# Kernel tuning notes

Measured on AMD Instinct MI355X. Metric: run time of the kernel, lower is better.

The kernel has to match this reference:

```python
import jax, jax.numpy as jnp
import numpy as np

EMB = 1024
HEADS = 16
S = EMB // HEADS  # per-head dim


def setup_inputs() -> dict:
    key = jax.random.key(0)
    ks = jax.random.split(key, 6)
    x = jax.random.normal(ks[0], (4, 2048, EMB), dtype=jnp.float32)
    # torch nn.Linear(s, s, bias=False): weight [out, in], y = x @ W.T
    Wk = jax.random.normal(ks[1], (S, S), dtype=jnp.float32) * (1.0 / np.sqrt(S))
    Wq = jax.random.normal(ks[2], (S, S), dtype=jnp.float32) * (1.0 / np.sqrt(S))
    Wv = jax.random.normal(ks[3], (S, S), dtype=jnp.float32) * (1.0 / np.sqrt(S))
    # unifyHeads: Linear(heads*s, emb) with bias
    Wu = jax.random.normal(ks[4], (EMB, EMB), dtype=jnp.float32) * (1.0 / np.sqrt(EMB))
    bu = jax.random.normal(ks[5], (EMB,), dtype=jnp.float32) * 0.01
    return {"x": x, "Wk": Wk, "Wq": Wq, "Wv": Wv, "Wu": Wu, "bu": bu}


def reference(x, Wk, Wq, Wv, Wu, bu):
    b, t, e = x.shape
    h, s = HEADS, S
    x4 = x.reshape(b, t, h, s)
    # per-head narrow projections (y = x @ W.T)
    k = jnp.einsum('bths,os->bhto', x4, Wk)  # [b,h,t,s]
    q = jnp.einsum('bths,os->bhto', x4, Wq)
    v = jnp.einsum('bths,os->bhto', x4, Wv)
    scale = e ** 0.25
    q = q / scale
    k = k / scale
    dot = jnp.einsum('bhqs,bhks->bhqk', q, k)  # [b,h,t,t]
    attn = jax.nn.softmax(dot, axis=-1)
    out = jnp.einsum('bhqk,bhks->bhqs', attn, v)  # [b,h,t,s]
    out = out.transpose(0, 2, 1, 3).reshape(b, t, h * s)
    return out @ Wu.T + bu
```

## Files before the change

### kernel.cpp

```cpp
#include <hip/hip_runtime.h>
#include <hip/hip_bf16.h>

#define BB 4
#define TT 2048
#define HH 16
#define SS 64
#define EE 1024

typedef __attribute__((ext_vector_type(8))) short short8;
typedef __attribute__((ext_vector_type(4))) short short4v;
typedef __attribute__((ext_vector_type(4))) float float4v;
typedef unsigned long long ull;

__device__ inline short f2bf(float f) {
    union { __hip_bfloat16 h; short s; } u;
    u.h = __float2bfloat16(f);
    return u.s;
}

__device__ inline unsigned pack_bf(float lo, float hi) {
    return ((unsigned)(unsigned short)f2bf(hi) << 16) | (unsigned short)f2bf(lo);
}

__device__ inline unsigned pack_trunc(float lo, float hi) {
    unsigned a = __builtin_bit_cast(unsigned, lo);
    unsigned b = __builtin_bit_cast(unsigned, hi);
    return (b & 0xFFFF0000u) | (a >> 16);
}

__device__ inline float4v mfma16(short8 a, short8 b, float4v c) {
    return __builtin_amdgcn_mfma_f32_16x16x32_bf16(a, b, c, 0, 0, 0);
}

#define LDSP(p) ((__attribute__((address_space(3))) void*)(p))
#define GLBP(p) ((const __attribute__((address_space(1))) void*)(p))

__global__ __launch_bounds__(256) void k_qkv(
    const float* __restrict__ x, const float* __restrict__ Wk,
    const float* __restrict__ Wq, const float* __restrict__ Wv,
    short* __restrict__ qb, short* __restrict__ kb, short* __restrict__ vb)
{
    __shared__ __attribute__((aligned(16))) short lw[3][64][72];
    const int tid = threadIdx.x;
    const float sq = 0.21233045f;

    for (int i = 0; i < 12; i++) {
        int u = tid + 256 * i;
        int w = u >> 10;
        int rem = u & 1023;
        int row = rem >> 4;
        int col = (rem & 15) * 4;
        const float* Wp = (w == 0) ? Wk : ((w == 1) ? Wq : Wv);
        float4v f = *reinterpret_cast<const float4v*>(Wp + row * 64 + col);
        float sc = (w == 2) ? 1.0f : sq;
        short4v s4;
        s4.x = f2bf(f.x * sc); s4.y = f2bf(f.y * sc);
        s4.z = f2bf(f.z * sc); s4.w = f2bf(f.w * sc);
        *reinterpret_cast<short4v*>(&lw[w][row][col]) = s4;
    }
    __syncthreads();

    const int wave = tid >> 6, lane = tid & 63;
    const int quad = lane >> 4, m = lane & 15;

    for (int rg = 0; rg < 4; rg++) {
        const long r0 = (long)blockIdx.x * 256 + rg * 64 + wave * 16;
        const int bt = (int)(r0 >> 4);
        const int b = bt >> 11, t = bt & 2047;

        const float* xrow = x + (r0 + m) * 64;
        short8 af[2];
        for (int ks = 0; ks < 2; ks++) {
            float4v f0 = *reinterpret_cast<const float4v*>(xrow + ks * 32 + quad * 8);
            float4v f1 = *reinterpret_cast<const float4v*>(xrow + ks * 32 + quad * 8 + 4);
            short8 a;
            a[0] = f2bf(f0.x); a[1] = f2bf(f0.y); a[2] = f2bf(f0.z); a[3] = f2bf(f0.w);
            a[4] = f2bf(f1.x); a[5] = f2bf(f1.y); a[6] = f2bf(f1.z); a[7] = f2bf(f1.w);
            af[ks] = a;
        }

        const long tb = ((long)(b * 16 + m) * 2048 + t) * 64;
        for (int w = 0; w < 3; w++) {
            short* dst = (w == 0) ? kb : ((w == 1) ? qb : vb);
            for (int c = 0; c < 4; c++) {
                float4v acc = {0.f, 0.f, 0.f, 0.f};
                for (int ks = 0; ks < 2; ks++) {
                    short8 wf = *reinterpret_cast<const short8*>(&lw[w][c * 16 + m][ks * 32 + quad * 8]);
                    acc = mfma16(wf, af[ks], acc);
                }
                unsigned lo = pack_bf(acc[0], acc[1]);
                unsigned hi = pack_bf(acc[2], acc[3]);
                ull wq = (ull)lo | ((ull)hi << 32);
                *reinterpret_cast<ull*>(dst + tb + c * 16 + quad * 4) = wq;
            }
        }
    }
}

__global__ __launch_bounds__(256) void k_prep(
    const short* __restrict__ vb, short* __restrict__ vtb,
    const float* __restrict__ Wu, short* __restrict__ wub)
{
    __shared__ short lt[64][65];
    const int bid = blockIdx.x;
    const int tid = threadIdx.x;
    if (bid < 2048) {
        int bh = bid >> 5, tb = bid & 31;
        const short* src = vb + ((long)bh * 2048 + tb * 64) * 64;
        for (int i = 0; i < 2; i++) {
            int u = tid + 256 * i;
            int row = u >> 3, seg = u & 7;
            short8 d = *reinterpret_cast<const short8*>(src + row * 64 + seg * 8);
            for (int j = 0; j < 8; j++) lt[seg * 8 + j][row] = d[j];
        }
        __syncthreads();
        short* dst = vtb + (long)bh * 64 * 2048 + tb * 64;
        for (int i = 0; i < 2; i++) {
            int u = tid + 256 * i;
            int srow = u >> 3, seg = u & 7;
            short8 d;
            for (int j = 0; j < 8; j++) d[j] = lt[srow][seg * 8 + j];
            *reinterpret_cast<short8*>(dst + (long)srow * 2048 + seg * 8) = d;
        }
    } else {
        int cb = bid - 2048;
        long base = (long)cb * 4096;
        for (int i = 0; i < 4; i++) {
            long e = base + (long)tid * 4 + (long)i * 1024;
            float4v f = *reinterpret_cast<const float4v*>(Wu + e);
            short4v s;
            s.x = f2bf(f.x); s.y = f2bf(f.y); s.z = f2bf(f.z); s.w = f2bf(f.w);
            *reinterpret_cast<short4v*>(wub + e) = s;
        }
    }
}

__global__ __launch_bounds__(256, 2) void k_attn(
    const short* __restrict__ qb, const short* __restrict__ kb,
    const short* __restrict__ vtb, short* __restrict__ ob)
{
    __shared__ __attribute__((aligned(16))) short kt_s[2][4096];
    __shared__ __attribute__((aligned(16))) short vt_s[2][4096];

    const int tid = threadIdx.x;
    const int wave = tid >> 6, lane = tid & 63;
    const int quad = lane >> 4, m = lane & 15;
    const int qblk = blockIdx.x, bh = blockIdx.y;
    const int q0 = qblk * 256;
    const long qoff = (long)bh * 2048 * 64;

    const short* kbase = kb + qoff;
    const short* vtbase = vtb + (long)bh * 64 * 2048;

    short8 qf[4][2];
    for (int sub = 0; sub < 4; sub++) {
        const short* qrow = qb + qoff + (long)(q0 + wave * 64 + sub * 16 + m) * 64;
        qf[sub][0] = *reinterpret_cast<const short8*>(qrow + quad * 8);
        qf[sub][1] = *reinterpret_cast<const short8*>(qrow + 32 + quad * 8);
    }

    float l[4] = {0.f, 0.f, 0.f, 0.f};
    float4v oacc[4][4];
    for (int s = 0; s < 4; s++)
        for (int c = 0; c < 4; c++) oacc[s][c] = (float4v){0.f, 0.f, 0.f, 0.f};

    for (int i = 0; i < 2; i++) {
        int u = i * 256 + tid;
        int row = u >> 3;
        int cb = (u & 7) ^ (row & 7);
        const short* gp = kbase + (long)row * 64 + cb * 8;
        short* lp = &kt_s[0][(i * 256 + wave * 64) * 8];
        __builtin_amdgcn_global_load_lds(GLBP(gp), LDSP(lp), 16, 0, 0);
    }
    for (int i = 0; i < 2; i++) {
        int g = i * 256 + tid;
        int d = g >> 3, a = g & 7;
        union { short8 v; ull u[2]; } uv;
        uv.v = *reinterpret_cast<const short8*>(vtbase + (long)d * 2048 + a * 8);
        for (int h = 0; h < 2; h++) {
            int key0 = a * 8 + 4 * h;
            int c = key0 >> 4, qk = (key0 >> 2) & 3;
            int kk = (c >> 1) * 32 + qk * 8 + (c & 1) * 4;
            int idx = d * 64 + (((kk >> 3) ^ (d & 7)) * 8) + (kk & 7);
            *reinterpret_cast<ull*>(&vt_s[0][idx]) = uv.u[h];
        }
    }

    int p = 0;
    for (int kt = 0; kt < 32; kt++) {
        __syncthreads();

        const bool pref = (kt < 31);
        union { short8 v; ull u[2]; } vreg[2];
        if (pref) {
            for (int i = 0; i < 2; i++) {
                int u = i * 256 + tid;
                int row = u >> 3;
                int cb = (u & 7) ^ (row & 7);
                const short* gp = kbase + (long)((kt + 1) * 64 + row) * 64 + cb * 8;
                short* lp = &kt_s[p ^ 1][(i * 256 + wave * 64) * 8];
                __builtin_amdgcn_global_load_lds(GLBP(gp), LDSP(lp), 16, 0, 0);
            }
            for (int i = 0; i < 2; i++) {
                int g = i * 256 + tid;
                int d = g >> 3, a = g & 7;
                vreg[i].v = *reinterpret_cast<const short8*>(
                    vtbase + (long)d * 2048 + (kt + 1) * 64 + a * 8);
            }
        }

        short8 kf[4][2];
        for (int c = 0; c < 4; c++)
            for (int ks = 0; ks < 2; ks++)
                kf[c][ks] = *reinterpret_cast<const short8*>(
                    &kt_s[p][(c * 16 + m) * 64 + (((ks * 4 + quad) ^ (m & 7)) * 8)]);

        float4v st[4][4];
        for (int sub = 0; sub < 4; sub++)
            for (int c = 0; c < 4; c++) {
                float4v z = {0.f, 0.f, 0.f, 0.f};
                z = mfma16(kf[c][0], qf[sub][0], z);
                st[sub][c] = mfma16(kf[c][1], qf[sub][1], z);
            }

        short8 vfr[4][2];
        for (int c2 = 0; c2 < 4; c2++)
            for (int ks = 0; ks < 2; ks++)
                vfr[c2][ks] = *reinterpret_cast<const short8*>(
                    &vt_s[p][(c2 * 16 + m) * 64 + (((ks * 4 + quad) ^ (m & 7)) * 8)]);

        for (int sub = 0; sub < 4; sub++) {
            __attribute__((aligned(16))) unsigned pp[8];
            for (int c = 0; c < 4; c++) {
                float e0 = __builtin_amdgcn_exp2f(st[sub][c][0]);
                float e1 = __builtin_amdgcn_exp2f(st[sub][c][1]);
                float e2 = __builtin_amdgcn_exp2f(st[sub][c][2]);
                float e3 = __builtin_amdgcn_exp2f(st[sub][c][3]);
                pp[c * 2]     = pack_trunc(e0, e1);
                pp[c * 2 + 1] = pack_trunc(e2, e3);
            }
            float ls = 0.f;
            for (int i = 0; i < 8; i++) {
                float flo = __builtin_bit_cast(float, pp[i] << 16);
                float fhi = __builtin_bit_cast(float, pp[i] & 0xFFFF0000u);
                ls += flo + fhi;
            }
            l[sub] += ls;
            const short8* pf = reinterpret_cast<const short8*>(pp);
            for (int ks = 0; ks < 2; ks++)
                for (int c2 = 0; c2 < 4; c2++)
                    oacc[sub][c2] = mfma16(vfr[c2][ks], pf[ks], oacc[sub][c2]);
        }

        if (pref) {
            for (int i = 0; i < 2; i++) {
                int g = i * 256 + tid;
                int d = g >> 3, a = g & 7;
                for (int h = 0; h < 2; h++) {
                    int key0 = a * 8 + 4 * h;
                    int c = key0 >> 4, qk = (key0 >> 2) & 3;
                    int kk = (c >> 1) * 32 + qk * 8 + (c & 1) * 4;
                    int idx = d * 64 + (((kk >> 3) ^ (d & 7)) * 8) + (kk & 7);
                    *reinterpret_cast<ull*>(&vt_s[p ^ 1][idx]) = vreg[i].u[h];
                }
            }
        }
        p ^= 1;
    }

    const int b = bh >> 4, h = bh & 15;
    for (int sub = 0; sub < 4; sub++) {
        float lv = l[sub];
        lv += __shfl_xor(lv, 16);
        lv += __shfl_xor(lv, 32);
        float li = 1.0f / lv;
        int t = q0 + wave * 64 + sub * 16 + m;
        long rowbase = (((long)(b * 2048 + t)) * 16 + h) * 64;
        for (int c2 = 0; c2 < 4; c2++) {
            unsigned w0 = pack_bf(oacc[sub][c2][0] * li, oacc[sub][c2][1] * li);
            unsigned w1 = pack_bf(oacc[sub][c2][2] * li, oacc[sub][c2][3] * li);
            ull wq = (ull)w0 | ((ull)w1 << 32);
            *reinterpret_cast<ull*>(ob + rowbase + c2 * 16 + quad * 4) = wq;
        }
    }
}

__global__ __launch_bounds__(256) void k_out(
    const short* __restrict__ ob, const short* __restrict__ wub,
    const float* __restrict__ bu, float* __restrict__ y)
{
    __shared__ __attribute__((aligned(16))) short a_s[2][8192];
    __shared__ __attribute__((aligned(16))) short b_s[2][8192];

    const int tid = threadIdx.x;
    const int wave = tid >> 6, lane = tid & 63;
    const int quad = lane >> 4, m = lane & 15;
    const int nb = blockIdx.x, mb = blockIdx.y;
    const long mbase = (long)mb * 128;
    const int nbase = nb * 128;
    const int wm = (wave & 1) * 64, wn = (wave >> 1) * 64;

    float4v acc[4][4];
    for (int i = 0; i < 4; i++)
        for (int j = 0; j < 4; j++) acc[i][j] = (float4v){0.f, 0.f, 0.f, 0.f};

    for (int i = 0; i < 4; i++) {
        int u = i * 256 + tid;
        int row = u >> 3;
        int c = (u & 7) ^ (row & 7);
        const short* gpA = ob + (mbase + row) * 1024 + c * 8;
        const short* gpB = wub + (long)(nbase + row) * 1024 + c * 8;
        short* lpA = &a_s[0][(i * 256 + wave * 64) * 8];
        short* lpB = &b_s[0][(i * 256 + wave * 64) * 8];
        __builtin_amdgcn_global_load_lds(GLBP(gpA), LDSP(lpA), 16, 0, 0);
        __builtin_amdgcn_global_load_lds(GLBP(gpB), LDSP(lpB), 16, 0, 0);
    }

    int p = 0;
    for (int kt = 0; kt < 16; kt++) {
        __syncthreads();
        if (kt < 15) {
            for (int i = 0; i < 4; i++) {
                int u = i * 256 + tid;
                int row = u >> 3;
                int c = (u & 7) ^ (row & 7);
                const short* gpA = ob + (mbase + row) * 1024 + (kt + 1) * 64 + c * 8;
                const short* gpB = wub + (long)(nbase + row) * 1024 + (kt + 1) * 64 + c * 8;
                short* lpA = &a_s[p ^ 1][(i * 256 + wave * 64) * 8];
                short* lpB = &b_s[p ^ 1][(i * 256 + wave * 64) * 8];
                __builtin_amdgcn_global_load_lds(GLBP(gpA), LDSP(lpA), 16, 0, 0);
                __builtin_amdgcn_global_load_lds(GLBP(gpB), LDSP(lpB), 16, 0, 0);
            }
        }
        for (int ks = 0; ks < 2; ks++) {
            short8 af[4], bf[4];
            for (int i = 0; i < 4; i++)
                af[i] = *reinterpret_cast<const short8*>(
                    &a_s[p][(wm + i * 16 + m) * 64 + (((ks * 4 + quad) ^ (m & 7)) * 8)]);
            for (int j = 0; j < 4; j++)
                bf[j] = *reinterpret_cast<const short8*>(
                    &b_s[p][(wn + j * 16 + m) * 64 + (((ks * 4 + quad) ^ (m & 7)) * 8)]);
            for (int i = 0; i < 4; i++)
                for (int j = 0; j < 4; j++)
                    acc[i][j] = mfma16(af[i], bf[j], acc[i][j]);
        }
        p ^= 1;
    }

    for (int j = 0; j < 4; j++) {
        int o = nbase + wn + j * 16 + m;
        float bias = bu[o];
        for (int i = 0; i < 4; i++) {
            for (int r = 0; r < 4; r++) {
                long row = mbase + wm + i * 16 + quad * 4 + r;
                y[row * 1024 + o] = acc[i][j][r] + bias;
            }
        }
    }
}

extern "C" void kernel_launch(void* const* d_in, const int* in_sizes, int n_in,
                              void* d_out, int out_size, void* d_ws, size_t ws_size,
                              hipStream_t stream)
{
    const float* x  = (const float*)d_in[0];
    const float* Wk = (const float*)d_in[1];
    const float* Wq = (const float*)d_in[2];
    const float* Wv = (const float*)d_in[3];
    const float* Wu = (const float*)d_in[4];
    const float* bu = (const float*)d_in[5];
    float* y = (float*)d_out;

    char* ws = (char*)d_ws;
    const size_t SEG = 16777216;
    short* qb  = (short*)(ws);
    short* kb  = (short*)(ws + 1 * SEG);
    short* vb  = (short*)(ws + 2 * SEG);
    short* vtb = (short*)(ws + 3 * SEG);
    short* ob  = (short*)(ws + 4 * SEG);
    short* wub = (short*)(ws + 5 * SEG);

    hipLaunchKernelGGL(k_qkv, dim3(512), dim3(256), 0, stream, x, Wk, Wq, Wv, qb, kb, vb);
    hipLaunchKernelGGL(k_prep, dim3(2304), dim3(256), 0, stream, vb, vtb, Wu, wub);
    hipLaunchKernelGGL(k_attn, dim3(8, 64), dim3(256), 0, stream, qb, kb, vtb, ob);
    hipLaunchKernelGGL(k_out, dim3(8, 64), dim3(256), 0, stream, ob, wub, bu, y);
}
```

Before: 216.0 us.

## Store QKV in token-major layout, compute softmax row sums via MFMA

The projection kernel now writes K, Q and V in a [b,t,h,s] token-major layout, so each wave's stores are contiguous 128-byte rows instead of strided per-head writes. The attention and transpose kernels read with a 1024-element row stride to match. In attention, the softmax denominator is accumulated with an extra MFMA against a ones vector instead of scalar unpack-and-add plus cross-lane shuffles. The QK^T scores are also computed per sub-tile to reduce register pressure. The trade-off is strided K/Q/V reads in attention and two extra MFMAs per sub-tile.

```diff
diff --git a/kernel.cpp b/kernel.cpp
--- a/kernel.cpp
+++ b/kernel.cpp
@@ -66,7 +66,6 @@
     for (int rg = 0; rg < 4; rg++) {
         const long r0 = (long)blockIdx.x * 256 + rg * 64 + wave * 16;
         const int bt = (int)(r0 >> 4);
-        const int b = bt >> 11, t = bt & 2047;
 
         const float* xrow = x + (r0 + m) * 64;
         short8 af[2];
@@ -79,7 +78,7 @@
             af[ks] = a;
         }
 
-        const long tb = ((long)(b * 16 + m) * 2048 + t) * 64;
+        const long tbase = (long)bt * 1024 + m * 64;
         for (int w = 0; w < 3; w++) {
             short* dst = (w == 0) ? kb : ((w == 1) ? qb : vb);
             for (int c = 0; c < 4; c++) {
@@ -91,7 +90,7 @@
                 unsigned lo = pack_bf(acc[0], acc[1]);
                 unsigned hi = pack_bf(acc[2], acc[3]);
                 ull wq = (ull)lo | ((ull)hi << 32);
-                *reinterpret_cast<ull*>(dst + tb + c * 16 + quad * 4) = wq;
+                *reinterpret_cast<ull*>(dst + tbase + c * 16 + quad * 4) = wq;
             }
         }
     }
@@ -106,11 +105,12 @@
     const int tid = threadIdx.x;
     if (bid < 2048) {
         int bh = bid >> 5, tb = bid & 31;
-        const short* src = vb + ((long)bh * 2048 + tb * 64) * 64;
+        int b = bh >> 4, h = bh & 15;
+        const short* src = vb + ((long)(b * 2048 + tb * 64)) * 1024 + h * 64;
         for (int i = 0; i < 2; i++) {
             int u = tid + 256 * i;
             int row = u >> 3, seg = u & 7;
-            short8 d = *reinterpret_cast<const short8*>(src + row * 64 + seg * 8);
+            short8 d = *reinterpret_cast<const short8*>(src + (long)row * 1024 + seg * 8);
             for (int j = 0; j < 8; j++) lt[seg * 8 + j][row] = d[j];
         }
         __syncthreads();
@@ -147,28 +147,32 @@
     const int quad = lane >> 4, m = lane & 15;
     const int qblk = blockIdx.x, bh = blockIdx.y;
     const int q0 = qblk * 256;
-    const long qoff = (long)bh * 2048 * 64;
-
-    const short* kbase = kb + qoff;
+    const int b = bh >> 4, h = bh & 15;
+
+    const short* kbase = kb + (long)b * 2048 * 1024 + h * 64;
     const short* vtbase = vtb + (long)bh * 64 * 2048;
 
     short8 qf[4][2];
     for (int sub = 0; sub < 4; sub++) {
-        const short* qrow = qb + qoff + (long)(q0 + wave * 64 + sub * 16 + m) * 64;
+        const short* qrow = qb + ((long)(b * 2048 + q0 + wave * 64 + sub * 16 + m)) * 1024 + h * 64;
         qf[sub][0] = *reinterpret_cast<const short8*>(qrow + quad * 8);
         qf[sub][1] = *reinterpret_cast<const short8*>(qrow + 32 + quad * 8);
     }
 
-    float l[4] = {0.f, 0.f, 0.f, 0.f};
+    const short8 ones = (short8)((short)0x3F80);
+
+    float4v lacc[4];
     float4v oacc[4][4];
-    for (int s = 0; s < 4; s++)
+    for (int s = 0; s < 4; s++) {
+        lacc[s] = (float4v){0.f, 0.f, 0.f, 0.f};
         for (int c = 0; c < 4; c++) oacc[s][c] = (float4v){0.f, 0.f, 0.f, 0.f};
+    }
 
     for (int i = 0; i < 2; i++) {
         int u = i * 256 + tid;
         int row = u >> 3;
         int cb = (u & 7) ^ (row & 7);
-        const short* gp = kbase + (long)row * 64 + cb * 8;
+        const short* gp = kbase + (long)row * 1024 + cb * 8;
         short* lp = &kt_s[0][(i * 256 + wave * 64) * 8];
         __builtin_amdgcn_global_load_lds(GLBP(gp), LDSP(lp), 16, 0, 0);
     }
@@ -177,12 +181,12 @@
         int d = g >> 3, a = g & 7;
         union { short8 v; ull u[2]; } uv;
         uv.v = *reinterpret_cast<const short8*>(vtbase + (long)d * 2048 + a * 8);
-        for (int h = 0; h < 2; h++) {
-            int key0 = a * 8 + 4 * h;
+        for (int hh = 0; hh < 2; hh++) {
+            int key0 = a * 8 + 4 * hh;
             int c = key0 >> 4, qk = (key0 >> 2) & 3;
             int kk = (c >> 1) * 32 + qk * 8 + (c & 1) * 4;
             int idx = d * 64 + (((kk >> 3) ^ (d & 7)) * 8) + (kk & 7);
-            *reinterpret_cast<ull*>(&vt_s[0][idx]) = uv.u[h];
+            *reinterpret_cast<ull*>(&vt_s[0][idx]) = uv.u[hh];
         }
     }
 
@@ -197,7 +201,7 @@
                 int u = i * 256 + tid;
                 int row = u >> 3;
                 int cb = (u & 7) ^ (row & 7);
-                const short* gp = kbase + (long)((kt + 1) * 64 + row) * 64 + cb * 8;
+                const short* gp = kbase + (long)((kt + 1) * 64 + row) * 1024 + cb * 8;
                 short* lp = &kt_s[p ^ 1][(i * 256 + wave * 64) * 8];
                 __builtin_amdgcn_global_load_lds(GLBP(gp), LDSP(lp), 16, 0, 0);
             }
@@ -209,44 +213,35 @@
             }
         }
 
-        short8 kf[4][2];
+        short8 kf[4][2], vfr[4][2];
         for (int c = 0; c < 4; c++)
             for (int ks = 0; ks < 2; ks++)
                 kf[c][ks] = *reinterpret_cast<const short8*>(
                     &kt_s[p][(c * 16 + m) * 64 + (((ks * 4 + quad) ^ (m & 7)) * 8)]);
-
-        float4v st[4][4];
-        for (int sub = 0; sub < 4; sub++)
-            for (int c = 0; c < 4; c++) {
-                float4v z = {0.f, 0.f, 0.f, 0.f};
-                z = mfma16(kf[c][0], qf[sub][0], z);
-                st[sub][c] = mfma16(kf[c][1], qf[sub][1], z);
-            }
-
-        short8 vfr[4][2];
         for (int c2 = 0; c2 < 4; c2++)
             for (int ks = 0; ks < 2; ks++)
                 vfr[c2][ks] = *reinterpret_cast<const short8*>(
                     &vt_s[p][(c2 * 16 + m) * 64 + (((ks * 4 + quad) ^ (m & 7)) * 8)]);
 
         for (int sub = 0; sub < 4; sub++) {
+            float4v st[4];
+            for (int c = 0; c < 4; c++) {
+                float4v z = {0.f, 0.f, 0.f, 0.f};
+                z = mfma16(kf[c][0], qf[sub][0], z);
+                st[c] = mfma16(kf[c][1], qf[sub][1], z);
+            }
             __attribute__((aligned(16))) unsigned pp[8];
             for (int c = 0; c < 4; c++) {
-                float e0 = __builtin_amdgcn_exp2f(st[sub][c][0]);
-                float e1 = __builtin_amdgcn_exp2f(st[sub][c][1]);
-                float e2 = __builtin_amdgcn_exp2f(st[sub][c][2]);
-                float e3 = __builtin_amdgcn_exp2f(st[sub][c][3]);
+                float e0 = __builtin_amdgcn_exp2f(st[c][0]);
+                float e1 = __builtin_amdgcn_exp2f(st[c][1]);
+                float e2 = __builtin_amdgcn_exp2f(st[c][2]);
+                float e3 = __builtin_amdgcn_exp2f(st[c][3]);
                 pp[c * 2]     = pack_trunc(e0, e1);
                 pp[c * 2 + 1] = pack_trunc(e2, e3);
             }
-            float ls = 0.f;
-            for (int i = 0; i < 8; i++) {
-                float flo = __builtin_bit_cast(float, pp[i] << 16);
-                float fhi = __builtin_bit_cast(float, pp[i] & 0xFFFF0000u);
-                ls += flo + fhi;
-            }
-            l[sub] += ls;
             const short8* pf = reinterpret_cast<const short8*>(pp);
+            lacc[sub] = mfma16(ones, pf[0], lacc[sub]);
+            lacc[sub] = mfma16(ones, pf[1], lacc[sub]);
             for (int ks = 0; ks < 2; ks++)
                 for (int c2 = 0; c2 < 4; c2++)
                     oacc[sub][c2] = mfma16(vfr[c2][ks], pf[ks], oacc[sub][c2]);
@@ -256,24 +251,20 @@
             for (int i = 0; i < 2; i++) {
                 int g = i * 256 + tid;
                 int d = g >> 3, a = g & 7;
-                for (int h = 0; h < 2; h++) {
-                    int key0 = a * 8 + 4 * h;
+                for (int hh = 0; hh < 2; hh++) {
+                    int key0 = a * 8 + 4 * hh;
                     int c = key0 >> 4, qk = (key0 >> 2) & 3;
                     int kk = (c >> 1) * 32 + qk * 8 + (c & 1) * 4;
                     int idx = d * 64 + (((kk >> 3) ^ (d & 7)) * 8) + (kk & 7);
-                    *reinterpret_cast<ull*>(&vt_s[p ^ 1][idx]) = vreg[i].u[h];
+                    *reinterpret_cast<ull*>(&vt_s[p ^ 1][idx]) = vreg[i].u[hh];
                 }
             }
         }
         p ^= 1;
     }
 
-    const int b = bh >> 4, h = bh & 15;
     for (int sub = 0; sub < 4; sub++) {
-        float lv = l[sub];
-        lv += __shfl_xor(lv, 16);
-        lv += __shfl_xor(lv, 32);
-        float li = 1.0f / lv;
+        float li = 1.0f / lacc[sub][0];
         int t = q0 + wave * 64 + sub * 16 + m;
         long rowbase = (((long)(b * 2048 + t)) * 16 + h) * 64;
         for (int c2 = 0; c2 < 4; c2++) {
```

Result: faster. 211.1 us (-2.3%).
